# Optimization experiments

Hardware: AMD Instinct MI355X
Metric: run time of the kernel (lower is better)

## Reference

```python
import jax, jax.numpy as jnp
import numpy as np

N_LAYERS = 3


def setup_inputs() -> dict:
    key = jax.random.key(0)
    k1, k2, k3, k4, k5, k6 = jax.random.split(key, 6)
    n_users, n_items, d = 100000, 50000, 64
    N = n_users + n_items
    nnz = 6400000
    user_emb = jax.random.normal(k1, (n_users, d), dtype=jnp.float32) * 0.1
    item_emb = jax.random.normal(k2, (n_items, d), dtype=jnp.float32) * 0.1
    # symmetric-normalized adjacency values are positive floats; random stand-in
    adj_data = jax.random.uniform(k3, (nnz,), dtype=jnp.float32) * 0.01
    adj_indices = jax.random.randint(k4, (nnz, 2), 0, N, dtype=jnp.int64)
    user_idx = jax.random.randint(k5, (4096,), 0, n_users, dtype=jnp.int64)
    item_idx = jax.random.randint(k6, (4096,), 0, n_items, dtype=jnp.int64)
    return {
        "user_emb": user_emb,
        "item_emb": item_emb,
        "adj_data": adj_data,
        "adj_indices": adj_indices,
        "user_idx": user_idx,
        "item_idx": item_idx,
    }


def _spmm(adj_data, rows, cols, e, N):
    # sparse (N,N) @ dense (N,d): gather cols, scale, scatter-add to rows
    msg = adj_data[:, None] * e[cols]          # (nnz, d)
    return jax.ops.segment_sum(msg, rows, num_segments=N)


def reference(user_emb, item_emb, adj_data, adj_indices, user_idx, item_idx):
    n_users = user_emb.shape[0]
    N = n_users + item_emb.shape[0]
    rows = adj_indices[:, 0]
    cols = adj_indices[:, 1]
    e_k = jnp.concatenate([user_emb, item_emb], axis=0)   # E^(0), (N, d)
    acc = e_k
    for _ in range(N_LAYERS):
        e_k = _spmm(adj_data, rows, cols, e_k, N)
        acc = acc + e_k
    e_final = acc / jnp.asarray(N_LAYERS + 1, e_k.dtype)  # mean over K+1 layers
    u = e_final[user_idx]                                  # (B, d)
    i = e_final[n_users + item_idx]                        # (B, d)
    return jnp.sum(u * i, axis=-1)                         # logits (B,)
```

## Files before the change

kernel.cpp:

```cpp
#include <hip/hip_runtime.h>


constexpr int D = 64;
constexpr int RB = 64;
constexpr int BCAP = 4096;
constexpr int CHUNK = 8192;

__device__ __forceinline__ float bflo(unsigned u) { return __uint_as_float(u << 16); }
__device__ __forceinline__ float bfhi(unsigned u) { return __uint_as_float(u & 0xFFFF0000u); }
__device__ __forceinline__ float bf1(ushort u) { return __uint_as_float((unsigned)u << 16); }
__device__ __forceinline__ unsigned bfpack(float f0, float f1) {
    unsigned u0 = __float_as_uint(f0), u1 = __float_as_uint(f1);
    u0 = (u0 + 0x7FFFu + ((u0 >> 16) & 1u)) >> 16;
    u1 = (u1 + 0x7FFFu + ((u1 >> 16) & 1u)) >> 16;
    return u0 | (u1 << 16);
}

__global__ __launch_bounds__(256) void pack_e0(const float4* __restrict__ u4,
                                               const float4* __restrict__ i4,
                                               uint2* __restrict__ ebf2,
                                               long long nU4, long long total4) {
    long long t = (long long)blockIdx.x * blockDim.x + threadIdx.x;
    if (t >= total4) return;
    float4 v = (t < nU4) ? u4[t] : i4[t - nU4];
    ebf2[t] = make_uint2(bfpack(v.x, v.y), bfpack(v.z, v.w));
}

__global__ __launch_bounds__(64) void gather_init(const float* __restrict__ ue,
                                                  const float* __restrict__ ie,
                                                  const int* __restrict__ uidx,
                                                  const int* __restrict__ iidx,
                                                  float* __restrict__ accU,
                                                  float* __restrict__ accI) {
    int j = blockIdx.x;
    int lane = threadIdx.x;
    accU[(size_t)j * D + lane] = ue[(size_t)uidx[j] * D + lane];
    accI[(size_t)j * D + lane] = ie[(size_t)iidx[j] * D + lane];
}

__global__ __launch_bounds__(256) void bin_scatter(const int2* __restrict__ idx2,
                                                   const float* __restrict__ adj,
                                                   int* __restrict__ cursor,
                                                   int2* __restrict__ binned,
                                                   long long nnz, int NB) {
    extern __shared__ int sh[];
    int* h = sh;
    int* rbase = sh + NB;
    const int tid = threadIdx.x;
    for (int i = tid; i < NB; i += 256) h[i] = 0;
    __syncthreads();
    const long long base = (long long)blockIdx.x * CHUNK;
    const bool full = (base + CHUNK <= nnz);

    if (full) {
        #pragma unroll
        for (int bb = 0; bb < 2; ++bb) {
            long long g0 = base + bb * 4096 + tid * 16;
            int4 m[8];
            #pragma unroll
            for (int k = 0; k < 8; ++k) m[k] = *(const int4*)(idx2 + g0 + 2 * k);
            #pragma unroll
            for (int k = 0; k < 8; ++k) {
                atomicAdd(&h[m[k].x >> 6], 1);
                atomicAdd(&h[m[k].z >> 6], 1);
            }
        }
    } else {
        for (int i = tid; i < CHUNK; i += 256) {
            long long g = base + i;
            if (g < nnz) atomicAdd(&h[idx2[g].x >> 6], 1);
        }
    }
    __syncthreads();

    for (int i = tid; i < NB; i += 256) {
        int v = h[i];
        rbase[i] = v ? atomicAdd(&cursor[i], v) : 0;
        h[i] = 0;
    }
    __syncthreads();

    auto emit = [&](int row, int col, float w) {
        int b = row >> 6;
        int pos = rbase[b] + atomicAdd(&h[b], 1);
        if (pos < BCAP)
            binned[(size_t)b * BCAP + pos] =
                make_int2(((row & 63) << 18) | col, __float_as_int(w));
    };
    if (full) {
        #pragma unroll
        for (int bb = 0; bb < 2; ++bb) {
            long long g0 = base + bb * 4096 + tid * 16;
            int4 m[8];
            float4 w[4];
            #pragma unroll
            for (int k = 0; k < 8; ++k) m[k] = *(const int4*)(idx2 + g0 + 2 * k);
            #pragma unroll
            for (int k = 0; k < 4; ++k) w[k] = *(const float4*)(adj + g0 + 4 * k);
            #pragma unroll
            for (int k = 0; k < 8; ++k) {
                float wa = (k & 1) ? ((k & 2) ? w[k >> 1].z : w[k >> 1].x)
                                   : ((k & 2) ? w[k >> 1].z : w[k >> 1].x);
                (void)wa;
            }
            #pragma unroll
            for (int k = 0; k < 8; ++k) {
                int e0i = 2 * k, e1i = 2 * k + 1;
                float w0 = ((const float*)w)[e0i];
                float w1 = ((const float*)w)[e1i];
                emit(m[k].x, m[k].y, w0);
                emit(m[k].z, m[k].w, w1);
            }
        }
    } else {
        for (int i = tid; i < CHUNK; i += 256) {
            long long g = base + i;
            if (g < nnz) {
                int2 rc = idx2[g];
                emit(rc.x, rc.y, adj[g]);
            }
        }
    }
}

__global__ __launch_bounds__(256) void bin_sort(int2* __restrict__ binned,
                                                const int* __restrict__ cursor,
                                                int2* __restrict__ row_se,
                                                int N) {
    __shared__ int2 buf[BCAP];
    __shared__ int h[RB];
    __shared__ int lcur[RB];
    int b = blockIdx.x, tid = threadIdx.x;
    size_t bbase = (size_t)b * BCAP;
    int len = cursor[b];
    if (len > BCAP) len = BCAP;
    for (int i = tid; i < len; i += 256) buf[i] = binned[bbase + i];
    if (tid < RB) h[tid] = 0;
    __syncthreads();
    for (int i = tid; i < len; i += 256) atomicAdd(&h[(buf[i].x >> 18) & 63], 1);
    __syncthreads();
    if (tid < RB) {
        int v = h[tid];
        int incl = v;
        #pragma unroll
        for (int off = 1; off < RB; off <<= 1) {
            int t = __shfl_up(incl, off, 64);
            if (tid >= off) incl += t;
        }
        int excl = incl - v;
        lcur[tid] = excl;
        int row = b * RB + tid;
        if (row < N) row_se[row] = make_int2((int)bbase + excl, (int)bbase + excl + v);
    }
    __syncthreads();
    for (int i = tid; i < len; i += 256) {
        int2 p = buf[i];
        int rb = (p.x >> 18) & 63;
        int pos = atomicAdd(&lcur[rb], 1);
        binned[bbase + pos] = make_int2(p.x & 0x3FFFF, p.y);
    }
}

__global__ __launch_bounds__(256) void spmm_bf16(const int2* __restrict__ csr,
                                                 const int2* __restrict__ row_se,
                                                 const ushort* __restrict__ ebf,
                                                 ushort* __restrict__ ebf_next,
                                                 int N) {
    int tid = threadIdx.x;
    int row = blockIdx.x * 4 + (tid >> 6);
    if (row >= N) return;
    int lane = tid & 63, eg = lane >> 3, sub = lane & 7;
    int2 se = row_se[row];
    int s = se.x, len = se.y - se.x;
    float a0 = 0, a1 = 0, a2 = 0, a3 = 0, a4 = 0, a5 = 0, a6 = 0, a7 = 0;
    #pragma unroll 2
    for (int i = eg; i < len; i += 8) {
        int2 cw = csr[s + i];
        float w = __int_as_float(cw.y);
        uint4 v = *(const uint4*)(ebf + (size_t)cw.x * D + sub * 8);
        a0 += w * bflo(v.x); a1 += w * bfhi(v.x);
        a2 += w * bflo(v.y); a3 += w * bfhi(v.y);
        a4 += w * bflo(v.z); a5 += w * bfhi(v.z);
        a6 += w * bflo(v.w); a7 += w * bfhi(v.w);
    }
    #pragma unroll
    for (int off = 8; off < 64; off <<= 1) {
        a0 += __shfl_xor(a0, off, 64); a1 += __shfl_xor(a1, off, 64);
        a2 += __shfl_xor(a2, off, 64); a3 += __shfl_xor(a3, off, 64);
        a4 += __shfl_xor(a4, off, 64); a5 += __shfl_xor(a5, off, 64);
        a6 += __shfl_xor(a6, off, 64); a7 += __shfl_xor(a7, off, 64);
    }
    if (eg == 0) {
        uint4 pk = make_uint4(bfpack(a0, a1), bfpack(a2, a3), bfpack(a4, a5), bfpack(a6, a7));
        *(uint4*)(ebf_next + (size_t)row * D + sub * 8) = pk;
    }
}

__global__ __launch_bounds__(256) void spmm_query(const int2* __restrict__ csr,
                                                  const int2* __restrict__ row_se,
                                                  const ushort* __restrict__ ebf,
                                                  const int* __restrict__ uidx,
                                                  const int* __restrict__ iidx,
                                                  float* __restrict__ accU,
                                                  float* __restrict__ accI,
                                                  int n_users, int nq) {
    int tid = threadIdx.x;
    int vq = blockIdx.x * 4 + (tid >> 6);
    if (vq >= 2 * nq) return;
    int lane = tid & 63, eg = lane >> 3, sub = lane & 7;
    bool isU = vq < nq;
    int j = isU ? vq : vq - nq;
    int row = isU ? uidx[j] : n_users + iidx[j];
    int2 se = row_se[row];
    int s = se.x, len = se.y - se.x;
    float a0 = 0, a1 = 0, a2 = 0, a3 = 0, a4 = 0, a5 = 0, a6 = 0, a7 = 0;
    #pragma unroll 2
    for (int i = eg; i < len; i += 8) {
        int2 cw = csr[s + i];
        float w = __int_as_float(cw.y);
        uint4 v = *(const uint4*)(ebf + (size_t)cw.x * D + sub * 8);
        a0 += w * bflo(v.x); a1 += w * bfhi(v.x);
        a2 += w * bflo(v.y); a3 += w * bfhi(v.y);
        a4 += w * bflo(v.z); a5 += w * bfhi(v.z);
        a6 += w * bflo(v.w); a7 += w * bfhi(v.w);
    }
    #pragma unroll
    for (int off = 8; off < 64; off <<= 1) {
        a0 += __shfl_xor(a0, off, 64); a1 += __shfl_xor(a1, off, 64);
        a2 += __shfl_xor(a2, off, 64); a3 += __shfl_xor(a3, off, 64);
        a4 += __shfl_xor(a4, off, 64); a5 += __shfl_xor(a5, off, 64);
        a6 += __shfl_xor(a6, off, 64); a7 += __shfl_xor(a7, off, 64);
    }
    if (eg == 0) {
        float* acc = (isU ? accU : accI) + (size_t)j * D + sub * 8;
        float4* f4 = (float4*)acc;
        float4 c0 = f4[0], c1 = f4[1];
        f4[0] = make_float4(c0.x + a0, c0.y + a1, c0.z + a2, c0.w + a3);
        f4[1] = make_float4(c1.x + a4, c1.y + a5, c1.z + a6, c1.w + a7);
    }
}

__global__ __launch_bounds__(64) void gather_acc(const ushort* __restrict__ e,
                                                 const int* __restrict__ uidx,
                                                 const int* __restrict__ iidx,
                                                 float* __restrict__ accU,
                                                 float* __restrict__ accI,
                                                 int n_users) {
    int j = blockIdx.x;
    int lane = threadIdx.x;
    accU[(size_t)j * D + lane] += bf1(e[(size_t)uidx[j] * D + lane]);
    accI[(size_t)j * D + lane] += bf1(e[((size_t)n_users + iidx[j]) * D + lane]);
}

__global__ __launch_bounds__(64) void final_dot(const float* __restrict__ accU,
                                                const float* __restrict__ accI,
                                                float* __restrict__ out) {
    int j = blockIdx.x;
    int lane = threadIdx.x;
    float p = accU[(size_t)j * D + lane] * accI[(size_t)j * D + lane];
    #pragma unroll
    for (int off = 32; off > 0; off >>= 1) p += __shfl_down(p, off);
    if (lane == 0) out[j] = p * (1.0f / 16.0f);
}

extern "C" void kernel_launch(void* const* d_in, const int* in_sizes, int n_in,
                              void* d_out, int out_size, void* d_ws, size_t ws_size,
                              hipStream_t stream) {
    const float* user_emb = (const float*)d_in[0];
    const float* item_emb = (const float*)d_in[1];
    const float* adj_data = (const float*)d_in[2];
    const int* adj_indices = (const int*)d_in[3];
    const int* user_idx = (const int*)d_in[4];
    const int* item_idx = (const int*)d_in[5];
    float* out = (float*)d_out;

    const int n_users = in_sizes[0] / D;
    const int n_items = in_sizes[1] / D;
    const long long nnz = in_sizes[2];
    const int N = n_users + n_items;
    const int nq = in_sizes[4];
    const int NB = (N + RB - 1) / RB;

    char* p = (char*)d_ws;
    auto alloc = [&](size_t bytes) { char* q = p; p += (bytes + 255) & ~(size_t)255; return q; };
    ushort* ebf0 = (ushort*)alloc((size_t)N * D * sizeof(ushort));
    ushort* ebf1 = (ushort*)alloc((size_t)N * D * sizeof(ushort));
    float* accU = (float*)alloc((size_t)nq * D * sizeof(float));
    float* accI = (float*)alloc((size_t)nq * D * sizeof(float));
    int2* binned = (int2*)alloc((size_t)NB * BCAP * sizeof(int2));
    int* cursor = (int*)alloc((size_t)NB * sizeof(int));
    int2* row_se = (int2*)alloc((size_t)N * sizeof(int2));

    const int2* idx2 = (const int2*)adj_indices;
    const int nChunks = (int)((nnz + CHUNK - 1) / CHUNK);
    const size_t sh_bytes = (size_t)2 * NB * sizeof(int);

    {
        long long total4 = (long long)N * (D / 4);
        long long nU4 = (long long)n_users * (D / 4);
        pack_e0<<<(int)((total4 + 255) / 256), 256, 0, stream>>>(
            (const float4*)user_emb, (const float4*)item_emb, (uint2*)ebf0, nU4, total4);
    }
    gather_init<<<nq, 64, 0, stream>>>(user_emb, item_emb, user_idx, item_idx, accU, accI);

    hipMemsetAsync(cursor, 0, (size_t)NB * sizeof(int), stream);
    bin_scatter<<<nChunks, 256, sh_bytes, stream>>>(idx2, adj_data, cursor, binned, nnz, NB);
    bin_sort<<<NB, 256, 0, stream>>>(binned, cursor, row_se, N);

    ushort* ebc = ebf0;
    ushort* ebn = ebf1;
    const int spmm_blocks = (N + 3) / 4;
    for (int layer = 0; layer < 2; ++layer) {
        spmm_bf16<<<spmm_blocks, 256, 0, stream>>>(binned, row_se, ebc, ebn, N);
        gather_acc<<<nq, 64, 0, stream>>>(ebn, user_idx, item_idx, accU, accI, n_users);
        ushort* t = ebc; ebc = ebn; ebn = t;
    }

    spmm_query<<<(2 * nq + 3) / 4, 256, 0, stream>>>(binned, row_se, ebc, user_idx, item_idx,
                                                     accU, accI, n_users, nq);

    final_dot<<<nq, 64, 0, stream>>>(accU, accI, out);
}
```

Measured before the change: 383.6 us.

## Replace shared-memory histogram binning with direct padded global atomics

The bin_scatter kernel drops its two-pass shared-memory histogram over all NB bins (about 2344 bins, so roughly 19KB of LDS per block) along with the per-block global reservation step. Each edge now takes its slot with a global atomicAdd on a cursor array padded to 16 ints per bin to avoid contention on shared cache lines. Chunk size falls to 4096 edges per block. This removes the LDS clearing, the extra index pass and the block barriers, but it issues 6.4M global atomics instead of far fewer per-block reservations, which risks atomic throughput limits.

```diff
diff --git a/kernel.cpp b/kernel.cpp
--- a/kernel.cpp
+++ b/kernel.cpp
@@ -4,7 +4,9 @@
 constexpr int D = 64;
 constexpr int RB = 64;
 constexpr int BCAP = 4096;
-constexpr int CHUNK = 8192;
+constexpr int EPT = 16;
+constexpr int CHUNK = 256 * EPT;
+constexpr int CPAD = 16;
 
 __device__ __forceinline__ float bflo(unsigned u) { return __uint_as_float(u << 16); }
 __device__ __forceinline__ float bfhi(unsigned u) { return __uint_as_float(u & 0xFFFF0000u); }
@@ -42,82 +44,46 @@
                                                    const float* __restrict__ adj,
                                                    int* __restrict__ cursor,
                                                    int2* __restrict__ binned,
-                                                   long long nnz, int NB) {
-    extern __shared__ int sh[];
-    int* h = sh;
-    int* rbase = sh + NB;
-    const int tid = threadIdx.x;
-    for (int i = tid; i < NB; i += 256) h[i] = 0;
-    __syncthreads();
-    const long long base = (long long)blockIdx.x * CHUNK;
-    const bool full = (base + CHUNK <= nnz);
-
-    if (full) {
-        #pragma unroll
-        for (int bb = 0; bb < 2; ++bb) {
-            long long g0 = base + bb * 4096 + tid * 16;
-            int4 m[8];
-            #pragma unroll
-            for (int k = 0; k < 8; ++k) m[k] = *(const int4*)(idx2 + g0 + 2 * k);
-            #pragma unroll
-            for (int k = 0; k < 8; ++k) {
-                atomicAdd(&h[m[k].x >> 6], 1);
-                atomicAdd(&h[m[k].z >> 6], 1);
-            }
+                                                   long long nnz) {
+    long long g0 = (long long)blockIdx.x * CHUNK + (long long)threadIdx.x * EPT;
+    if (g0 + EPT <= nnz) {
+        int4 m[EPT / 2];
+        float4 w[EPT / 4];
+        #pragma unroll
+        for (int k = 0; k < EPT / 2; ++k) m[k] = *(const int4*)(idx2 + g0 + 2 * k);
+        #pragma unroll
+        for (int k = 0; k < EPT / 4; ++k) w[k] = *(const float4*)(adj + g0 + 4 * k);
+        int pos[EPT], bin[EPT];
+        #pragma unroll
+        for (int k = 0; k < EPT / 2; ++k) {
+            bin[2 * k]     = m[k].x >> 6;
+            bin[2 * k + 1] = m[k].z >> 6;
+        }
+        #pragma unroll
+        for (int k = 0; k < EPT; ++k)
+            pos[k] = atomicAdd(&cursor[bin[k] * CPAD], 1);
+        #pragma unroll
+        for (int k = 0; k < EPT / 2; ++k) {
+            int p0 = pos[2 * k], p1 = pos[2 * k + 1];
+            if (p0 < BCAP)
+                binned[(size_t)bin[2 * k] * BCAP + p0] =
+                    make_int2(((m[k].x & 63) << 18) | m[k].y,
+                              __float_as_int(((const float*)w)[2 * k]));
+            if (p1 < BCAP)
+                binned[(size_t)bin[2 * k + 1] * BCAP + p1] =
+                    make_int2(((m[k].z & 63) << 18) | m[k].w,
+                              __float_as_int(((const float*)w)[2 * k + 1]));
         }
     } else {
-        for (int i = tid; i < CHUNK; i += 256) {
-            long long g = base + i;
-            if (g < nnz) atomicAdd(&h[idx2[g].x >> 6], 1);
-        }
-    }
-    __syncthreads();
-
-    for (int i = tid; i < NB; i += 256) {
-        int v = h[i];
-        rbase[i] = v ? atomicAdd(&cursor[i], v) : 0;
-        h[i] = 0;
-    }
-    __syncthreads();
-
-    auto emit = [&](int row, int col, float w) {
-        int b = row >> 6;
-        int pos = rbase[b] + atomicAdd(&h[b], 1);
-        if (pos < BCAP)
-            binned[(size_t)b * BCAP + pos] =
-                make_int2(((row & 63) << 18) | col, __float_as_int(w));
-    };
-    if (full) {
-        #pragma unroll
-        for (int bb = 0; bb < 2; ++bb) {
-            long long g0 = base + bb * 4096 + tid * 16;
-            int4 m[8];
-            float4 w[4];
-            #pragma unroll
-            for (int k = 0; k < 8; ++k) m[k] = *(const int4*)(idx2 + g0 + 2 * k);
-            #pragma unroll
-            for (int k = 0; k < 4; ++k) w[k] = *(const float4*)(adj + g0 + 4 * k);
-            #pragma unroll
-            for (int k = 0; k < 8; ++k) {
-                float wa = (k & 1) ? ((k & 2) ? w[k >> 1].z : w[k >> 1].x)
-                                   : ((k & 2) ? w[k >> 1].z : w[k >> 1].x);
-                (void)wa;
-            }
-            #pragma unroll
-            for (int k = 0; k < 8; ++k) {
-                int e0i = 2 * k, e1i = 2 * k + 1;
-                float w0 = ((const float*)w)[e0i];
-                float w1 = ((const float*)w)[e1i];
-                emit(m[k].x, m[k].y, w0);
-                emit(m[k].z, m[k].w, w1);
-            }
-        }
-    } else {
-        for (int i = tid; i < CHUNK; i += 256) {
-            long long g = base + i;
+        for (int i = 0; i < EPT; ++i) {
+            long long g = g0 + i;
             if (g < nnz) {
                 int2 rc = idx2[g];
-                emit(rc.x, rc.y, adj[g]);
+                int b = rc.x >> 6;
+                int pos = atomicAdd(&cursor[b * CPAD], 1);
+                if (pos < BCAP)
+                    binned[(size_t)b * BCAP + pos] =
+                        make_int2(((rc.x & 63) << 18) | rc.y, __float_as_int(adj[g]));
             }
         }
     }
@@ -132,7 +98,7 @@
     __shared__ int lcur[RB];
     int b = blockIdx.x, tid = threadIdx.x;
     size_t bbase = (size_t)b * BCAP;
-    int len = cursor[b];
+    int len = cursor[b * CPAD];
     if (len > BCAP) len = BCAP;
     for (int i = tid; i < len; i += 256) buf[i] = binned[bbase + i];
     if (tid < RB) h[tid] = 0;
@@ -288,12 +254,11 @@
     float* accU = (float*)alloc((size_t)nq * D * sizeof(float));
     float* accI = (float*)alloc((size_t)nq * D * sizeof(float));
     int2* binned = (int2*)alloc((size_t)NB * BCAP * sizeof(int2));
-    int* cursor = (int*)alloc((size_t)NB * sizeof(int));
+    int* cursor = (int*)alloc((size_t)NB * CPAD * sizeof(int));
     int2* row_se = (int2*)alloc((size_t)N * sizeof(int2));
 
     const int2* idx2 = (const int2*)adj_indices;
     const int nChunks = (int)((nnz + CHUNK - 1) / CHUNK);
-    const size_t sh_bytes = (size_t)2 * NB * sizeof(int);
 
     {
         long long total4 = (long long)N * (D / 4);
@@ -303,8 +268,8 @@
     }
     gather_init<<<nq, 64, 0, stream>>>(user_emb, item_emb, user_idx, item_idx, accU, accI);
 
-    hipMemsetAsync(cursor, 0, (size_t)NB * sizeof(int), stream);
-    bin_scatter<<<nChunks, 256, sh_bytes, stream>>>(idx2, adj_data, cursor, binned, nnz, NB);
+    hipMemsetAsync(cursor, 0, (size_t)NB * CPAD * sizeof(int), stream);
+    bin_scatter<<<nChunks, 256, 0, stream>>>(idx2, adj_data, cursor, binned, nnz);
     bin_sort<<<NB, 256, 0, stream>>>(binned, cursor, row_se, N);
 
     ushort* ebc = ebf0;
```

New measurement: 680.5 us. 77.4% more time.

## Replace single-pass row binning with two-level super-bin then fine-bin scatter

Applied to the files above, without the earlier changes.

Replaces the single scatter into about 2344 fine row bins with two passes. The first pass scatters edges into 37 super-bins of 4096 rows each, using a small LDS histogram. The second pass splits each super-bin into 64 fine bins. Per-block global cursor atomics drop and write locality improves, at the cost of an extra read and write of all edges. The workspace now aliases the super-bin buffer with later buffers, and the fine-bin capacity drops to 3072, which risks truncating rows if a bin overflows.

```diff
diff --git a/kernel.cpp b/kernel.cpp
--- a/kernel.cpp
+++ b/kernel.cpp
@@ -3,8 +3,13 @@
 
 constexpr int D = 64;
 constexpr int RB = 64;
-constexpr int BCAP = 4096;
+constexpr int BCAP = 3072;
+constexpr int SRB = 4096;
+constexpr int SCAP = 180224;
+constexpr int SCHUNK = 8192;
+constexpr int CPS = SCAP / SCHUNK;
 constexpr int CHUNK = 8192;
+constexpr int SB_MAX = 64;
 
 __device__ __forceinline__ float bflo(unsigned u) { return __uint_as_float(u << 16); }
 __device__ __forceinline__ float bfhi(unsigned u) { return __uint_as_float(u & 0xFFFF0000u); }
@@ -38,16 +43,15 @@
     accI[(size_t)j * D + lane] = ie[(size_t)iidx[j] * D + lane];
 }
 
-__global__ __launch_bounds__(256) void bin_scatter(const int2* __restrict__ idx2,
-                                                   const float* __restrict__ adj,
-                                                   int* __restrict__ cursor,
-                                                   int2* __restrict__ binned,
-                                                   long long nnz, int NB) {
-    extern __shared__ int sh[];
-    int* h = sh;
-    int* rbase = sh + NB;
+__global__ __launch_bounds__(256) void scatter_super(const int2* __restrict__ idx2,
+                                                     const float* __restrict__ adj,
+                                                     int* __restrict__ scur,
+                                                     int2* __restrict__ sbinned,
+                                                     long long nnz, int nsup) {
+    __shared__ int h[SB_MAX];
+    __shared__ int rbase[SB_MAX];
     const int tid = threadIdx.x;
-    for (int i = tid; i < NB; i += 256) h[i] = 0;
+    if (tid < nsup) h[tid] = 0;
     __syncthreads();
     const long long base = (long long)blockIdx.x * CHUNK;
     const bool full = (base + CHUNK <= nnz);
@@ -55,42 +59,40 @@
     if (full) {
         #pragma unroll
         for (int bb = 0; bb < 2; ++bb) {
-            long long g0 = base + bb * 4096 + tid * 16;
+            long long g0 = base + bb * 4096 + (long long)tid * 16;
             int4 m[8];
             #pragma unroll
             for (int k = 0; k < 8; ++k) m[k] = *(const int4*)(idx2 + g0 + 2 * k);
             #pragma unroll
             for (int k = 0; k < 8; ++k) {
-                atomicAdd(&h[m[k].x >> 6], 1);
-                atomicAdd(&h[m[k].z >> 6], 1);
+                atomicAdd(&h[m[k].x >> 12], 1);
+                atomicAdd(&h[m[k].z >> 12], 1);
             }
         }
     } else {
         for (int i = tid; i < CHUNK; i += 256) {
             long long g = base + i;
-            if (g < nnz) atomicAdd(&h[idx2[g].x >> 6], 1);
-        }
-    }
-    __syncthreads();
-
-    for (int i = tid; i < NB; i += 256) {
-        int v = h[i];
-        rbase[i] = v ? atomicAdd(&cursor[i], v) : 0;
-        h[i] = 0;
-    }
-    __syncthreads();
-
+            if (g < nnz) atomicAdd(&h[idx2[g].x >> 12], 1);
+        }
+    }
+    __syncthreads();
+    if (tid < nsup) {
+        int v = h[tid];
+        rbase[tid] = v ? atomicAdd(&scur[tid], v) : 0;
+        h[tid] = 0;
+    }
+    __syncthreads();
     auto emit = [&](int row, int col, float w) {
-        int b = row >> 6;
-        int pos = rbase[b] + atomicAdd(&h[b], 1);
-        if (pos < BCAP)
-            binned[(size_t)b * BCAP + pos] =
-                make_int2(((row & 63) << 18) | col, __float_as_int(w));
+        int s = row >> 12;
+        int pos = rbase[s] + atomicAdd(&h[s], 1);
+        if (pos < SCAP)
+            sbinned[(size_t)s * SCAP + pos] =
+                make_int2(((row & (SRB - 1)) << 18) | col, __float_as_int(w));
     };
     if (full) {
         #pragma unroll
         for (int bb = 0; bb < 2; ++bb) {
-            long long g0 = base + bb * 4096 + tid * 16;
+            long long g0 = base + bb * 4096 + (long long)tid * 16;
             int4 m[8];
             float4 w[4];
             #pragma unroll
@@ -99,17 +101,8 @@
             for (int k = 0; k < 4; ++k) w[k] = *(const float4*)(adj + g0 + 4 * k);
             #pragma unroll
             for (int k = 0; k < 8; ++k) {
-                float wa = (k & 1) ? ((k & 2) ? w[k >> 1].z : w[k >> 1].x)
-                                   : ((k & 2) ? w[k >> 1].z : w[k >> 1].x);
-                (void)wa;
-            }
-            #pragma unroll
-            for (int k = 0; k < 8; ++k) {
-                int e0i = 2 * k, e1i = 2 * k + 1;
-                float w0 = ((const float*)w)[e0i];
-                float w1 = ((const float*)w)[e1i];
-                emit(m[k].x, m[k].y, w0);
-                emit(m[k].z, m[k].w, w1);
+                emit(m[k].x, m[k].y, ((const float*)w)[2 * k]);
+                emit(m[k].z, m[k].w, ((const float*)w)[2 * k + 1]);
             }
         }
     } else {
@@ -119,6 +112,76 @@
                 int2 rc = idx2[g];
                 emit(rc.x, rc.y, adj[g]);
             }
+        }
+    }
+}
+
+__global__ __launch_bounds__(256) void scatter_fine(const int2* __restrict__ sbinned,
+                                                    const int* __restrict__ scount,
+                                                    int* __restrict__ cursor,
+                                                    int2* __restrict__ binned) {
+    __shared__ int h[64];
+    __shared__ int rbase[64];
+    const int tid = threadIdx.x;
+    const int s = blockIdx.x / CPS;
+    const int c = blockIdx.x % CPS;
+    int len = scount[s];
+    if (len > SCAP) len = SCAP;
+    const int begin = c * SCHUNK;
+    const int end = min(begin + SCHUNK, len);
+    if (begin >= end) return;
+    if (tid < 64) h[tid] = 0;
+    __syncthreads();
+    const int2* src = sbinned + (size_t)s * SCAP;
+    const bool full = (end - begin == SCHUNK);
+
+    if (full) {
+        #pragma unroll
+        for (int bb = 0; bb < 2; ++bb) {
+            int g0 = begin + bb * 4096 + tid * 16;
+            int4 m[8];
+            #pragma unroll
+            for (int k = 0; k < 8; ++k) m[k] = *(const int4*)(src + g0 + 2 * k);
+            #pragma unroll
+            for (int k = 0; k < 8; ++k) {
+                atomicAdd(&h[(m[k].x >> 24) & 63], 1);
+                atomicAdd(&h[(m[k].z >> 24) & 63], 1);
+            }
+        }
+    } else {
+        for (int i = begin + tid; i < end; i += 256)
+            atomicAdd(&h[(src[i].x >> 24) & 63], 1);
+    }
+    __syncthreads();
+    if (tid < 64) {
+        int v = h[tid];
+        rbase[tid] = v ? atomicAdd(&cursor[s * 64 + tid], v) : 0;
+        h[tid] = 0;
+    }
+    __syncthreads();
+    auto emit = [&](int x, int wbits) {
+        int f = (x >> 24) & 63;
+        int pos = rbase[f] + atomicAdd(&h[f], 1);
+        if (pos < BCAP)
+            binned[(size_t)(s * 64 + f) * BCAP + pos] = make_int2(x & 0xFFFFFF, wbits);
+    };
+    if (full) {
+        #pragma unroll
+        for (int bb = 0; bb < 2; ++bb) {
+            int g0 = begin + bb * 4096 + tid * 16;
+            int4 m[8];
+            #pragma unroll
+            for (int k = 0; k < 8; ++k) m[k] = *(const int4*)(src + g0 + 2 * k);
+            #pragma unroll
+            for (int k = 0; k < 8; ++k) {
+                emit(m[k].x, m[k].y);
+                emit(m[k].z, m[k].w);
+            }
+        }
+    } else {
+        for (int i = begin + tid; i < end; i += 256) {
+            int2 e = src[i];
+            emit(e.x, e.y);
         }
     }
 }
@@ -280,20 +343,34 @@
     const int N = n_users + n_items;
     const int nq = in_sizes[4];
     const int NB = (N + RB - 1) / RB;
+    const int nsup = (N + SRB - 1) / SRB;
+    const int NBF = nsup * 64;
 
     char* p = (char*)d_ws;
     auto alloc = [&](size_t bytes) { char* q = p; p += (bytes + 255) & ~(size_t)255; return q; };
     ushort* ebf0 = (ushort*)alloc((size_t)N * D * sizeof(ushort));
-    ushort* ebf1 = (ushort*)alloc((size_t)N * D * sizeof(ushort));
-    float* accU = (float*)alloc((size_t)nq * D * sizeof(float));
-    float* accI = (float*)alloc((size_t)nq * D * sizeof(float));
-    int2* binned = (int2*)alloc((size_t)NB * BCAP * sizeof(int2));
-    int* cursor = (int*)alloc((size_t)NB * sizeof(int));
-    int2* row_se = (int2*)alloc((size_t)N * sizeof(int2));
+    int2* binned = (int2*)alloc((size_t)NBF * BCAP * sizeof(int2));
+    char* uni = p;
+    {
+        size_t tail = 0;
+        tail += ((size_t)N * D * sizeof(ushort) + 255) & ~(size_t)255;
+        tail += 2 * (((size_t)nq * D * sizeof(float) + 255) & ~(size_t)255);
+        tail += ((size_t)N * sizeof(int2) + 255) & ~(size_t)255;
+        size_t sb = ((size_t)nsup * SCAP * sizeof(int2) + 255) & ~(size_t)255;
+        p += (sb > tail ? sb : tail);
+    }
+    int2* sbinned = (int2*)uni;
+    char* q = uni;
+    auto suballoc = [&](size_t bytes) { char* r = q; q += (bytes + 255) & ~(size_t)255; return r; };
+    ushort* ebf1 = (ushort*)suballoc((size_t)N * D * sizeof(ushort));
+    float* accU = (float*)suballoc((size_t)nq * D * sizeof(float));
+    float* accI = (float*)suballoc((size_t)nq * D * sizeof(float));
+    int2* row_se = (int2*)suballoc((size_t)N * sizeof(int2));
+    int* cursor = (int*)alloc((size_t)NBF * sizeof(int));
+    int* scur = (int*)alloc((size_t)SB_MAX * sizeof(int));
 
     const int2* idx2 = (const int2*)adj_indices;
-    const int nChunks = (int)((nnz + CHUNK - 1) / CHUNK);
-    const size_t sh_bytes = (size_t)2 * NB * sizeof(int);
+    const int nChunksA1 = (int)((nnz + CHUNK - 1) / CHUNK);
 
     {
         long long total4 = (long long)N * (D / 4);
@@ -301,11 +378,14 @@
         pack_e0<<<(int)((total4 + 255) / 256), 256, 0, stream>>>(
             (const float4*)user_emb, (const float4*)item_emb, (uint2*)ebf0, nU4, total4);
     }
+
+    hipMemsetAsync(scur, 0, (size_t)SB_MAX * sizeof(int), stream);
+    hipMemsetAsync(cursor, 0, (size_t)NBF * sizeof(int), stream);
+    scatter_super<<<nChunksA1, 256, 0, stream>>>(idx2, adj_data, scur, sbinned, nnz, nsup);
+    scatter_fine<<<nsup * CPS, 256, 0, stream>>>(sbinned, scur, cursor, binned);
+    bin_sort<<<NB, 256, 0, stream>>>(binned, cursor, row_se, N);
+
     gather_init<<<nq, 64, 0, stream>>>(user_emb, item_emb, user_idx, item_idx, accU, accI);
-
-    hipMemsetAsync(cursor, 0, (size_t)NB * sizeof(int), stream);
-    bin_scatter<<<nChunks, 256, sh_bytes, stream>>>(idx2, adj_data, cursor, binned, nnz, NB);
-    bin_sort<<<NB, 256, 0, stream>>>(binned, cursor, row_se, N);
 
     ushort* ebc = ebf0;
     ushort* ebn = ebf1;
```

Result: faster. 371.8 us (-3.1%).
